# Kernel tuning notes

Measured on AMD Instinct MI355X. Metric: run time of the kernel, lower is better.

Reference implementation:

```python
import jax, jax.numpy as jnp
import numpy as np

NUM_NEIGHBORS = 10
BN_EPS = 1e-5


def setup_inputs() -> dict:
    key = jax.random.key(0)
    ks = jax.random.split(key, 6)
    B, N, D = 8, 4096, 64
    x = jax.random.normal(ks[0], (B, N, D), jnp.float32)

    def w(k, shape):
        return jax.random.normal(k, shape, jnp.float32) * 0.05

    return {
        "x": x,
        "gamma": jnp.ones((D,), jnp.float32),
        "beta": jnp.zeros((D,), jnp.float32),
        "W1": w(ks[1], (128, 128)), "b1": jnp.zeros((128,), jnp.float32),
        "W2": w(ks[2], (128, 64)), "b2": jnp.zeros((64,), jnp.float32),
        "W3": w(ks[3], (64, 64)), "b3": jnp.zeros((64,), jnp.float32),
        "Wg": w(ks[4], (128, 64)), "bg": jnp.zeros((64,), jnp.float32),
    }


def reference(x, gamma, beta, W1, b1, W2, b2, W3, b3, Wg, bg):
    B, N, D = x.shape
    K = NUM_NEIGHBORS

    # BatchNorm1d in train mode: normalize over all B*N rows with batch stats
    xf = x.reshape(-1, D)
    mu = jnp.mean(xf, axis=0)
    var = jnp.mean((xf - mu) ** 2, axis=0)  # biased, as torch BN uses
    xn = (((xf - mu) / jnp.sqrt(var + BN_EPS)) * gamma + beta).reshape(B, N, D)

    # KNN in feature space (standard DGCNN gather_neighbours)
    sq = jnp.sum(xn * xn, axis=-1)  # [B,N]
    dist = sq[:, :, None] + sq[:, None, :] - 2.0 * jnp.einsum("bnd,bmd->bnm", xn, xn)
    _, idx = jax.lax.top_k(-dist, K)  # [B,N,K] indices of nearest (incl. self)

    # gather neighbor features: neigh[b,n,k,:] = xn[b, idx[b,n,k], :]
    neigh = jax.vmap(lambda f, i: f[i])(xn, idx)  # [B,N,K,D]

    exp = jnp.broadcast_to(xn[:, :, None, :], (B, N, K, D))
    edge = jnp.concatenate([exp, exp - neigh], axis=-1)  # [B,N,K,2D]

    h = jax.nn.relu(edge @ W1 + b1)
    h = jax.nn.relu(h @ W2 + b2)
    h = jax.nn.relu(h @ W3 + b3)  # [B,N,K,64]

    vert = jnp.max(h, axis=2)  # max over neighbors -> [B,N,64]
    g = jnp.max(vert, axis=1, keepdims=True)  # global max-pool [B,1,64]
    cat = jnp.concatenate([vert, jnp.broadcast_to(g, vert.shape)], axis=-1)  # [B,N,128]
    return jax.nn.relu(cat @ Wg + bg)  # [B,N,64]
```

## Files before the change

### kernel.cpp

```cpp
#include <hip/hip_runtime.h>
#include <hip/hip_fp16.h>
#include <float.h>

#define BB 8
#define NN 4096
#define DD 64
#define KNBR 10
#define ROWS (BB*NN)

typedef _Float16 f16x8 __attribute__((ext_vector_type(8)));
typedef float f32x4 __attribute__((ext_vector_type(4)));

__global__ void k_bn_stats(const float* __restrict__ x, float* __restrict__ stats) {
  __shared__ float ls[2][4][64];
  int d = threadIdx.x & 63;
  int g = threadIdx.x >> 6;
  float s = 0.f, s2 = 0.f;
  for (int r = blockIdx.x * 4 + g; r < ROWS; r += gridDim.x * 4) {
    float val = x[r * 64 + d];
    s += val;
    s2 = fmaf(val, val, s2);
  }
  ls[0][g][d] = s;
  ls[1][g][d] = s2;
  __syncthreads();
  if (g == 0) {
    atomicAdd(&stats[d],      ls[0][0][d] + ls[0][1][d] + ls[0][2][d] + ls[0][3][d]);
    atomicAdd(&stats[64 + d], ls[1][0][d] + ls[1][1][d] + ls[1][2][d] + ls[1][3][d]);
  }
}

__global__ void k_bn_finalize(const float* __restrict__ stats,
                              const float* __restrict__ gamma,
                              const float* __restrict__ beta,
                              float* __restrict__ ss) {
  int d = threadIdx.x;
  const float inv = 1.f / 32768.f;
  float mu  = stats[d] * inv;
  float var = stats[64 + d] * inv - mu * mu;
  float sc  = gamma[d] / sqrtf(var + 1e-5f);
  ss[d]      = sc;
  ss[64 + d] = beta[d] - mu * sc;
}

__global__ void k_normalize(const float* __restrict__ x, const float* __restrict__ ss,
                            float* __restrict__ xn, float* __restrict__ sq,
                            _Float16* __restrict__ xh, _Float16* __restrict__ xl) {
  int row = blockIdx.x * 4 + (threadIdx.x >> 6);
  int d = threadIdx.x & 63;
  int idx = row * 64 + d;
  float val = fmaf(x[idx], ss[d], ss[64 + d]);
  xn[idx] = val;
  _Float16 h = (_Float16)val;
  _Float16 l = (_Float16)(val - (float)h);
  xh[idx] = h;
  xl[idx] = l;
  float p = val * val;
  #pragma unroll
  for (int off = 32; off > 0; off >>= 1) p += __shfl_xor(p, off);
  if (d == 0) sq[row] = p;
}

__global__ __launch_bounds__(256, 2) void k_knn(const _Float16* __restrict__ xh,
                                                const _Float16* __restrict__ xl,
                                                const float* __restrict__ sq,
                                                int* __restrict__ knn) {
  __shared__ __align__(16) float lds[16640];
  __shared__ float thrs[64];
  __shared__ int cnts[64];
  const int tid = threadIdx.x;
  const int w = tid >> 6, lane = tid & 63;
  const int l15 = lane & 15, lg = lane >> 4;
  const int b = blockIdx.x >> 6;
  const int rowbase = (blockIdx.x & 63) << 6;
  const int bN = b * NN;
  const _Float16* __restrict__ xhb = xh + (size_t)bN * 64;
  const _Float16* __restrict__ xlb = xl + (size_t)bN * 64;

  char* wbase = (char*)lds + w * 16640;
  char* Bhi = wbase;
  char* Blo = wbase + 4096;
  float* Dw = (float*)(wbase + 8192);

  f16x8 Ah[4][2], Al[4][2];
  #pragma unroll
  for (int mt = 0; mt < 4; ++mt) {
    #pragma unroll
    for (int ks = 0; ks < 2; ++ks) {
      int r = rowbase + mt * 16 + l15;
      Ah[mt][ks] = *(const f16x8*)(xhb + r * 64 + ks * 32 + lg * 8);
      Al[mt][ks] = *(const f16x8*)(xlb + r * 64 + ks * 32 + lg * 8);
    }
  }

  float bd[10];
  #pragma unroll
  for (int i = 0; i < 10; ++i) bd[i] = FLT_MAX;

  int srow[4], scc[4];
  #pragma unroll
  for (int i = 0; i < 4; ++i) { int c = i * 64 + lane; srow[i] = c >> 3; scc[i] = c & 7; }

  f16x8 sh[4], sl[4];
  {
    int mb0 = w * 32;
    #pragma unroll
    for (int i = 0; i < 4; ++i) {
      sh[i] = *(const f16x8*)(xhb + (mb0 + srow[i]) * 64 + scc[i] * 8);
      sl[i] = *(const f16x8*)(xlb + (mb0 + srow[i]) * 64 + scc[i] * 8);
    }
  }

  float* Drow = Dw + lane * 33;

  #pragma unroll 1
  for (int t = 0; t < 32; ++t) {
    const int mb = (t * 4 + w) * 32;
    const int mb2 = (t < 31) ? ((t + 1) * 4 + w) * 32 : mb;
    float sqv0 = sq[bN + mb + l15];
    float sqv1 = sq[bN + mb + 16 + l15];
    #pragma unroll
    for (int i = 0; i < 4; ++i) {
      int off = srow[i] * 128 + 16 * (scc[i] ^ (srow[i] & 7));
      *(f16x8*)(Bhi + off) = sh[i];
      *(f16x8*)(Blo + off) = sl[i];
    }
    #pragma unroll
    for (int i = 0; i < 4; ++i) {
      sh[i] = *(const f16x8*)(xhb + (mb2 + srow[i]) * 64 + scc[i] * 8);
      sl[i] = *(const f16x8*)(xlb + (mb2 + srow[i]) * 64 + scc[i] * 8);
    }
    f16x8 Bh[2][2], Bl[2][2];
    #pragma unroll
    for (int nt = 0; nt < 2; ++nt) {
      #pragma unroll
      for (int ks = 0; ks < 2; ++ks) {
        int rr2 = nt * 16 + l15;
        int off = rr2 * 128 + 16 * ((ks * 4 + lg) ^ (rr2 & 7));
        Bh[nt][ks] = *(const f16x8*)(Bhi + off);
        Bl[nt][ks] = *(const f16x8*)(Blo + off);
      }
    }
    #pragma unroll
    for (int mt = 0; mt < 4; ++mt) {
      f32x4 a0 = {0.f, 0.f, 0.f, 0.f}, a1 = {0.f, 0.f, 0.f, 0.f};
      #pragma unroll
      for (int ks = 0; ks < 2; ++ks) {
        a0 = __builtin_amdgcn_mfma_f32_16x16x32_f16(Ah[mt][ks], Bh[0][ks], a0, 0, 0, 0);
        a1 = __builtin_amdgcn_mfma_f32_16x16x32_f16(Ah[mt][ks], Bh[1][ks], a1, 0, 0, 0);
        a0 = __builtin_amdgcn_mfma_f32_16x16x32_f16(Ah[mt][ks], Bl[0][ks], a0, 0, 0, 0);
        a1 = __builtin_amdgcn_mfma_f32_16x16x32_f16(Ah[mt][ks], Bl[1][ks], a1, 0, 0, 0);
        a0 = __builtin_amdgcn_mfma_f32_16x16x32_f16(Al[mt][ks], Bh[0][ks], a0, 0, 0, 0);
        a1 = __builtin_amdgcn_mfma_f32_16x16x32_f16(Al[mt][ks], Bh[1][ks], a1, 0, 0, 0);
      }
      int rw = mt * 16 + lg * 4;
      #pragma unroll
      for (int r2 = 0; r2 < 4; ++r2) {
        Dw[(rw + r2) * 33 + l15]      = fmaf(-2.f, a0[r2], sqv0);
        Dw[(rw + r2) * 33 + 16 + l15] = fmaf(-2.f, a1[r2], sqv1);
      }
    }
    #pragma unroll 4
    for (int mm = 0; mm < 32; ++mm) {
      float cd = Drow[mm];
      if (cd < bd[9]) {
        float prev = bd[0];
        bd[0] = fminf(cd, bd[0]);
        #pragma unroll
        for (int j = 1; j < 10; ++j) {
          float cur = bd[j];
          bd[j] = fminf(cur, fmaxf(prev, cd));
          prev = cur;
        }
      }
    }
  }

  __syncthreads();
  float* md = lds;
  #pragma unroll
  for (int i = 0; i < 10; ++i) md[(w * 64 + lane) * 10 + i] = bd[i];
  if (tid < 64) cnts[tid] = 0;
  __syncthreads();
  if (tid < 64) {
    float fd[10];
    #pragma unroll
    for (int i = 0; i < 10; ++i) fd[i] = FLT_MAX;
    for (int w2 = 0; w2 < 4; ++w2) {
      #pragma unroll
      for (int kk = 0; kk < 10; ++kk) {
        float cd = md[(w2 * 64 + tid) * 10 + kk];
        if (cd < fd[9]) {
          float prev = fd[0];
          fd[0] = fminf(cd, fd[0]);
          #pragma unroll
          for (int j = 1; j < 10; ++j) {
            float cur = fd[j];
            fd[j] = fminf(cur, fmaxf(prev, cd));
            prev = cur;
          }
        }
      }
    }
    thrs[tid] = fd[9];
  }
  __syncthreads();

  float thv[4][4];
  #pragma unroll
  for (int mt = 0; mt < 4; ++mt)
    #pragma unroll
    for (int r2 = 0; r2 < 4; ++r2)
      thv[mt][r2] = thrs[mt * 16 + lg * 4 + r2];

  int* knnrow = knn + (size_t)(bN + rowbase) * KNBR;

  {
    int mb0 = w * 32;
    #pragma unroll
    for (int i = 0; i < 4; ++i) {
      sh[i] = *(const f16x8*)(xhb + (mb0 + srow[i]) * 64 + scc[i] * 8);
      sl[i] = *(const f16x8*)(xlb + (mb0 + srow[i]) * 64 + scc[i] * 8);
    }
  }
  #pragma unroll 1
  for (int t = 0; t < 32; ++t) {
    const int mb = (t * 4 + w) * 32;
    const int mb2 = (t < 31) ? ((t + 1) * 4 + w) * 32 : mb;
    float sqv0 = sq[bN + mb + l15];
    float sqv1 = sq[bN + mb + 16 + l15];
    #pragma unroll
    for (int i = 0; i < 4; ++i) {
      int off = srow[i] * 128 + 16 * (scc[i] ^ (srow[i] & 7));
      *(f16x8*)(Bhi + off) = sh[i];
      *(f16x8*)(Blo + off) = sl[i];
    }
    #pragma unroll
    for (int i = 0; i < 4; ++i) {
      sh[i] = *(const f16x8*)(xhb + (mb2 + srow[i]) * 64 + scc[i] * 8);
      sl[i] = *(const f16x8*)(xlb + (mb2 + srow[i]) * 64 + scc[i] * 8);
    }
    f16x8 Bh[2][2], Bl[2][2];
    #pragma unroll
    for (int nt = 0; nt < 2; ++nt) {
      #pragma unroll
      for (int ks = 0; ks < 2; ++ks) {
        int rr2 = nt * 16 + l15;
        int off = rr2 * 128 + 16 * ((ks * 4 + lg) ^ (rr2 & 7));
        Bh[nt][ks] = *(const f16x8*)(Bhi + off);
        Bl[nt][ks] = *(const f16x8*)(Blo + off);
      }
    }
    #pragma unroll
    for (int mt = 0; mt < 4; ++mt) {
      f32x4 a0 = {0.f, 0.f, 0.f, 0.f}, a1 = {0.f, 0.f, 0.f, 0.f};
      #pragma unroll
      for (int ks = 0; ks < 2; ++ks) {
        a0 = __builtin_amdgcn_mfma_f32_16x16x32_f16(Ah[mt][ks], Bh[0][ks], a0, 0, 0, 0);
        a1 = __builtin_amdgcn_mfma_f32_16x16x32_f16(Ah[mt][ks], Bh[1][ks], a1, 0, 0, 0);
        a0 = __builtin_amdgcn_mfma_f32_16x16x32_f16(Ah[mt][ks], Bl[0][ks], a0, 0, 0, 0);
        a1 = __builtin_amdgcn_mfma_f32_16x16x32_f16(Ah[mt][ks], Bl[1][ks], a1, 0, 0, 0);
        a0 = __builtin_amdgcn_mfma_f32_16x16x32_f16(Al[mt][ks], Bh[0][ks], a0, 0, 0, 0);
        a1 = __builtin_amdgcn_mfma_f32_16x16x32_f16(Al[mt][ks], Bh[1][ks], a1, 0, 0, 0);
      }
      #pragma unroll
      for (int r2 = 0; r2 < 4; ++r2) {
        float d0 = fmaf(-2.f, a0[r2], sqv0);
        float d1 = fmaf(-2.f, a1[r2], sqv1);
        int row = mt * 16 + lg * 4 + r2;
        if (d0 <= thv[mt][r2]) {
          int slot = atomicAdd(&cnts[row], 1);
          if (slot < KNBR) knnrow[row * KNBR + slot] = bN + mb + l15;
        }
        if (d1 <= thv[mt][r2]) {
          int slot = atomicAdd(&cnts[row], 1);
          if (slot < KNBR) knnrow[row * KNBR + slot] = bN + mb + 16 + l15;
        }
      }
    }
  }
}

__global__ void k_uv(const float* __restrict__ xn, const float* __restrict__ W1,
                     const float* __restrict__ b1, _Float16* __restrict__ u,
                     _Float16* __restrict__ v) {
  __shared__ float xs[64 * 64];
  const int tid = threadIdx.x;
  const int o = tid & 127;
  const bool isU = tid < 128;
  const int rowbase = blockIdx.x * 64;

  float wreg[64];
  #pragma unroll
  for (int d = 0; d < 64; ++d) {
    float bw = W1[(64 + d) * 128 + o];
    wreg[d] = isU ? (W1[d * 128 + o] + bw) : bw;
  }
  const float bb = isU ? b1[o] : 0.f;
  _Float16* __restrict__ dst = isU ? u : v;

  {
    const float4* s4 = (const float4*)(xn + rowbase * 64);
    float4* d4 = (float4*)xs;
    #pragma unroll
    for (int i = 0; i < 4; ++i) d4[tid + 256 * i] = s4[tid + 256 * i];
  }
  __syncthreads();

  for (int r = 0; r < 64; ++r) {
    const float4* xr = (const float4*)(xs + r * 64);
    float a0 = bb, a1 = 0.f, a2 = 0.f, a3 = 0.f;
    #pragma unroll
    for (int q = 0; q < 16; ++q) {
      float4 xv = xr[q];
      a0 = fmaf(xv.x, wreg[4 * q + 0], a0);
      a1 = fmaf(xv.y, wreg[4 * q + 1], a1);
      a2 = fmaf(xv.z, wreg[4 * q + 2], a2);
      a3 = fmaf(xv.w, wreg[4 * q + 3], a3);
    }
    dst[(rowbase + r) * 128 + o] = (_Float16)((a0 + a1) + (a2 + a3));
  }
}

__global__ __launch_bounds__(256, 2) void k_edge(const _Float16* __restrict__ uu,
                                                 const _Float16* __restrict__ vv,
                                                 const int* __restrict__ knn,
                                                 const float* __restrict__ W2,
                                                 const float* __restrict__ b2,
                                                 const float* __restrict__ W3,
                                                 const float* __restrict__ b3,
                                                 float* __restrict__ vert) {
  __shared__ __align__(16) _Float16 W3Ts[64 * 72];
  __shared__ __align__(16) _Float16 h2buf[4][16 * 88];
  __shared__ int vmaxs[4][512];
  const int tid = threadIdx.x;
  const int w = tid >> 6, lane = tid & 63;
  const int l15 = lane & 15, lg = lane >> 4;

  for (int i = tid; i < 64 * 64; i += 256) {
    int o3 = i >> 6, k2 = i & 63;
    W3Ts[o3 * 72 + k2] = (_Float16)W3[k2 * 64 + o3];
  }
  f16x8 w2f[4][4];
  #pragma unroll
  for (int ks = 0; ks < 4; ++ks) {
    #pragma unroll
    for (int nt = 0; nt < 4; ++nt) {
      f16x8 t;
      #pragma unroll
      for (int j = 0; j < 8; ++j)
        t[j] = (_Float16)W2[(ks * 32 + lg * 8 + j) * 64 + nt * 16 + l15];
      w2f[ks][nt] = t;
    }
  }
  float bias2[4], bias3[4];
  #pragma unroll
  for (int nt = 0; nt < 4; ++nt) { bias2[nt] = b2[nt * 16 + l15]; bias3[nt] = b3[nt * 16 + l15]; }

  _Float16* h2w = h2buf[w];
  int* vmaxw = vmaxs[w];
  #pragma unroll
  for (int q = 0; q < 8; ++q) vmaxw[lane * 8 + q] = 0;
  __syncthreads();

  const int g = blockIdx.x * 4 + w;
  const int n0 = g * 8;
  const int ebase = n0 * KNBR;
  #pragma unroll 1
  for (int mt = 0; mt < 5; ++mt) {
    const int e = mt * 16 + l15;
    const int m = knn[ebase + e];
    const int n = n0 + e / 10;
    const _Float16* Up = uu + (size_t)n * 128 + lg * 8;
    const _Float16* Vp = vv + (size_t)m * 128 + lg * 8;
    f16x8 A[4];
    #pragma unroll
    for (int ks = 0; ks < 4; ++ks) {
      f16x8 ud = *(const f16x8*)(Up + ks * 32);
      f16x8 vd = *(const f16x8*)(Vp + ks * 32);
      f16x8 df = ud - vd;
      f16x8 t;
      #pragma unroll
      for (int j = 0; j < 8; ++j)
        t[j] = df[j] > (_Float16)0.f ? df[j] : (_Float16)0.f;
      A[ks] = t;
    }
    f32x4 acc[4];
    #pragma unroll
    for (int nt = 0; nt < 4; ++nt) { float bbv = bias2[nt]; acc[nt] = (f32x4){bbv, bbv, bbv, bbv}; }
    #pragma unroll
    for (int ks = 0; ks < 4; ++ks) {
      #pragma unroll
      for (int nt = 0; nt < 4; ++nt)
        acc[nt] = __builtin_amdgcn_mfma_f32_16x16x32_f16(A[ks], w2f[ks][nt], acc[nt], 0, 0, 0);
    }
    #pragma unroll
    for (int nt = 0; nt < 4; ++nt) {
      #pragma unroll
      for (int r = 0; r < 4; ++r)
        h2w[(lg * 4 + r) * 88 + nt * 16 + l15] = (_Float16)fmaxf(acc[nt][r], 0.f);
    }
    f16x8 A3[2];
    #pragma unroll
    for (int ks2 = 0; ks2 < 2; ++ks2)
      A3[ks2] = *(const f16x8*)(h2w + l15 * 88 + ks2 * 32 + lg * 8);
    f32x4 c3[4];
    #pragma unroll
    for (int nt = 0; nt < 4; ++nt) { float bbv = bias3[nt]; c3[nt] = (f32x4){bbv, bbv, bbv, bbv}; }
    #pragma unroll
    for (int ks2 = 0; ks2 < 2; ++ks2) {
      #pragma unroll
      for (int nt = 0; nt < 4; ++nt) {
        f16x8 bf = *(const f16x8*)(W3Ts + (nt * 16 + l15) * 72 + ks2 * 32 + lg * 8);
        c3[nt] = __builtin_amdgcn_mfma_f32_16x16x32_f16(A3[ks2], bf, c3[nt], 0, 0, 0);
      }
    }
    #pragma unroll
    for (int nt = 0; nt < 4; ++nt) {
      #pragma unroll
      for (int r = 0; r < 4; ++r) {
        float val = fmaxf(c3[nt][r], 0.f);
        int e2 = mt * 16 + lg * 4 + r;
        int p = e2 / 10;
        atomicMax(&vmaxw[p * 64 + nt * 16 + l15], __float_as_int(val));
      }
    }
  }
  {
    int p2 = lane >> 3, c0 = (lane & 7) * 8;
    const int* vp = &vmaxw[p2 * 64 + c0];
    float4 r0, r1;
    r0.x = __int_as_float(vp[0]); r0.y = __int_as_float(vp[1]);
    r0.z = __int_as_float(vp[2]); r0.w = __int_as_float(vp[3]);
    r1.x = __int_as_float(vp[4]); r1.y = __int_as_float(vp[5]);
    r1.z = __int_as_float(vp[6]); r1.w = __int_as_float(vp[7]);
    *(float4*)(vert + (size_t)(n0 + p2) * 64 + c0) = r0;
    *(float4*)(vert + (size_t)(n0 + p2) * 64 + c0 + 4) = r1;
  }
}

__global__ void k_gmax(const float* __restrict__ vert, float* __restrict__ g) {
  __shared__ float red[4][64];
  int b = blockIdx.x >> 4, chunk = blockIdx.x & 15;
  int sub = threadIdx.x >> 6, o = threadIdx.x & 63;
  float vm = 0.f;
  for (int j = 0; j < 64; ++j) {
    int r = chunk * 256 + j * 4 + sub;
    vm = fmaxf(vm, vert[(b * NN + r) * 64 + o]);
  }
  red[sub][o] = vm;
  __syncthreads();
  if (sub == 0) {
    float mm = fmaxf(fmaxf(red[0][o], red[1][o]), fmaxf(red[2][o], red[3][o]));
    atomicMax((int*)&g[b * 64 + o], __float_as_int(mm));
  }
}

__global__ void k_gb(const float* __restrict__ g, const float* __restrict__ Wg,
                     const float* __restrict__ bg, float* __restrict__ gb) {
  int t = threadIdx.x;
  int b = t >> 6, o = t & 63;
  float acc = bg[o];
  #pragma unroll
  for (int i = 0; i < 64; ++i)
    acc = fmaf(g[b * 64 + i], Wg[(64 + i) * 64 + o], acc);
  gb[b * 64 + o] = acc;
}

__global__ void k_final(const float* __restrict__ vert, const float* __restrict__ Wg,
                        const float* __restrict__ gb, float* __restrict__ out) {
  __shared__ float Wgs[64 * 64];
  int tid = threadIdx.x, w = tid >> 6, lane = tid & 63;
  for (int i = tid; i < 4096; i += 256) Wgs[i] = Wg[i];
  __syncthreads();
  int gw = blockIdx.x * 4 + w;
  for (int j = 0; j < 4; ++j) {
    int n = gw + 8192 * j;
    int b = n >> 12;
    float vrow = vert[n * 64 + lane];
    float ac0 = gb[b * 64 + lane], ac1 = 0.f, ac2 = 0.f, ac3 = 0.f;
    #pragma unroll
    for (int i = 0; i < 64; i += 4) {
      ac0 = fmaf(__shfl(vrow, i),     Wgs[i * 64 + lane],       ac0);
      ac1 = fmaf(__shfl(vrow, i + 1), Wgs[(i + 1) * 64 + lane], ac1);
      ac2 = fmaf(__shfl(vrow, i + 2), Wgs[(i + 2) * 64 + lane], ac2);
      ac3 = fmaf(__shfl(vrow, i + 3), Wgs[(i + 3) * 64 + lane], ac3);
    }
    out[n * 64 + lane] = fmaxf((ac0 + ac1) + (ac2 + ac3), 0.f);
  }
}

extern "C" void kernel_launch(void* const* d_in, const int* in_sizes, int n_in,
                              void* d_out, int out_size, void* d_ws, size_t ws_size,
                              hipStream_t stream) {
  const float* x     = (const float*)d_in[0];
  const float* gamma = (const float*)d_in[1];
  const float* beta  = (const float*)d_in[2];
  const float* W1    = (const float*)d_in[3];
  const float* b1    = (const float*)d_in[4];
  const float* W2    = (const float*)d_in[5];
  const float* b2    = (const float*)d_in[6];
  const float* W3    = (const float*)d_in[7];
  const float* b3    = (const float*)d_in[8];
  const float* Wg    = (const float*)d_in[9];
  const float* bg    = (const float*)d_in[10];
  float* out = (float*)d_out;

  float* ws    = (float*)d_ws;
  float* stats = ws;
  float* ss    = ws + 128;
  float* xn    = ws + 256;
  float* sq    = xn + 2097152;
  int*   knn   = (int*)(sq + 32768);
  _Float16* u  = (_Float16*)(knn + 327680);
  _Float16* v  = u + 4194304;
  float* vert  = (float*)(v + 4194304);
  float* g     = vert + 2097152;
  float* gb    = g + 512;
  _Float16* xh = (_Float16*)(gb + 512);
  _Float16* xl = (_Float16*)(gb + 512 + 1048576);

  hipMemsetAsync(stats, 0, 128 * sizeof(float), stream);
  hipMemsetAsync(g, 0, 512 * sizeof(float), stream);

  k_bn_stats<<<256, 256, 0, stream>>>(x, stats);
  k_bn_finalize<<<1, 64, 0, stream>>>(stats, gamma, beta, ss);
  k_normalize<<<8192, 256, 0, stream>>>(x, ss, xn, sq, xh, xl);
  k_knn<<<512, 256, 0, stream>>>(xh, xl, sq, knn);
  k_uv<<<512, 256, 0, stream>>>(xn, W1, b1, u, v);
  k_edge<<<1024, 256, 0, stream>>>(u, v, knn, W2, b2, W3, b3, vert);
  k_gmax<<<128, 256, 0, stream>>>(vert, g);
  k_gb<<<1, 512, 0, stream>>>(g, Wg, bg, gb);
  k_final<<<2048, 256, 0, stream>>>(vert, Wg, gb, out);
}
```

Before: 459.7 us.

## Fuse global max-pool into edge kernel and global bias into final kernel

The per-batch global max over vertex features is now reduced in shared memory inside the edge kernel and pushed with one atomicMax per channel per block, which removes the separate gmax kernel and its re-read of vert. The global-feature projection (g @ Wg bottom half + bg) is recomputed in every final-kernel block instead of in a dedicated single-block kernel. Two launches go away, at the cost of extra shared atomics in the edge kernel and 512x64 redundant FMAs per final block.

```diff
diff --git a/kernel.cpp b/kernel.cpp
--- a/kernel.cpp
+++ b/kernel.cpp
@@ -329,10 +329,12 @@
                                                  const float* __restrict__ b2,
                                                  const float* __restrict__ W3,
                                                  const float* __restrict__ b3,
-                                                 float* __restrict__ vert) {
+                                                 float* __restrict__ vert,
+                                                 float* __restrict__ gmax) {
   __shared__ __align__(16) _Float16 W3Ts[64 * 72];
   __shared__ __align__(16) _Float16 h2buf[4][16 * 88];
   __shared__ int vmaxs[4][512];
+  __shared__ int gblk[64];
   const int tid = threadIdx.x;
   const int w = tid >> 6, lane = tid & 63;
   const int l15 = lane & 15, lg = lane >> 4;
@@ -361,6 +363,7 @@
   int* vmaxw = vmaxs[w];
   #pragma unroll
   for (int q = 0; q < 8; ++q) vmaxw[lane * 8 + q] = 0;
+  if (tid < 64) gblk[tid] = 0;
   __syncthreads();
 
   const int g = blockIdx.x * 4 + w;
@@ -436,49 +439,44 @@
     r1.z = __int_as_float(vp[6]); r1.w = __int_as_float(vp[7]);
     *(float4*)(vert + (size_t)(n0 + p2) * 64 + c0) = r0;
     *(float4*)(vert + (size_t)(n0 + p2) * 64 + c0 + 4) = r1;
-  }
-}
-
-__global__ void k_gmax(const float* __restrict__ vert, float* __restrict__ g) {
-  __shared__ float red[4][64];
-  int b = blockIdx.x >> 4, chunk = blockIdx.x & 15;
-  int sub = threadIdx.x >> 6, o = threadIdx.x & 63;
-  float vm = 0.f;
-  for (int j = 0; j < 64; ++j) {
-    int r = chunk * 256 + j * 4 + sub;
-    vm = fmaxf(vm, vert[(b * NN + r) * 64 + o]);
-  }
-  red[sub][o] = vm;
-  __syncthreads();
-  if (sub == 0) {
-    float mm = fmaxf(fmaxf(red[0][o], red[1][o]), fmaxf(red[2][o], red[3][o]));
-    atomicMax((int*)&g[b * 64 + o], __float_as_int(mm));
-  }
-}
-
-__global__ void k_gb(const float* __restrict__ g, const float* __restrict__ Wg,
-                     const float* __restrict__ bg, float* __restrict__ gb) {
-  int t = threadIdx.x;
-  int b = t >> 6, o = t & 63;
-  float acc = bg[o];
-  #pragma unroll
-  for (int i = 0; i < 64; ++i)
-    acc = fmaf(g[b * 64 + i], Wg[(64 + i) * 64 + o], acc);
-  gb[b * 64 + o] = acc;
+    atomicMax(&gblk[c0 + 0], __float_as_int(r0.x));
+    atomicMax(&gblk[c0 + 1], __float_as_int(r0.y));
+    atomicMax(&gblk[c0 + 2], __float_as_int(r0.z));
+    atomicMax(&gblk[c0 + 3], __float_as_int(r0.w));
+    atomicMax(&gblk[c0 + 4], __float_as_int(r1.x));
+    atomicMax(&gblk[c0 + 5], __float_as_int(r1.y));
+    atomicMax(&gblk[c0 + 6], __float_as_int(r1.z));
+    atomicMax(&gblk[c0 + 7], __float_as_int(r1.w));
+  }
+  __syncthreads();
+  if (tid < 64) {
+    int bb2 = (blockIdx.x * 32) >> 12;
+    atomicMax((int*)&gmax[bb2 * 64 + tid], gblk[tid]);
+  }
 }
 
 __global__ void k_final(const float* __restrict__ vert, const float* __restrict__ Wg,
-                        const float* __restrict__ gb, float* __restrict__ out) {
+                        const float* __restrict__ bg, const float* __restrict__ gmax,
+                        float* __restrict__ out) {
   __shared__ float Wgs[64 * 64];
+  __shared__ float gbs[8 * 64];
   int tid = threadIdx.x, w = tid >> 6, lane = tid & 63;
   for (int i = tid; i < 4096; i += 256) Wgs[i] = Wg[i];
+  for (int t2 = tid; t2 < 512; t2 += 256) {
+    int b_ = t2 >> 6, o = t2 & 63;
+    float acc = bg[o];
+    #pragma unroll
+    for (int i = 0; i < 64; ++i)
+      acc = fmaf(gmax[b_ * 64 + i], Wg[(64 + i) * 64 + o], acc);
+    gbs[t2] = acc;
+  }
   __syncthreads();
   int gw = blockIdx.x * 4 + w;
   for (int j = 0; j < 4; ++j) {
     int n = gw + 8192 * j;
     int b = n >> 12;
     float vrow = vert[n * 64 + lane];
-    float ac0 = gb[b * 64 + lane], ac1 = 0.f, ac2 = 0.f, ac3 = 0.f;
+    float ac0 = gbs[b * 64 + lane], ac1 = 0.f, ac2 = 0.f, ac3 = 0.f;
     #pragma unroll
     for (int i = 0; i < 64; i += 4) {
       ac0 = fmaf(__shfl(vrow, i),     Wgs[i * 64 + lane],       ac0);
@@ -516,9 +514,8 @@
   _Float16* v  = u + 4194304;
   float* vert  = (float*)(v + 4194304);
   float* g     = vert + 2097152;
-  float* gb    = g + 512;
-  _Float16* xh = (_Float16*)(gb + 512);
-  _Float16* xl = (_Float16*)(gb + 512 + 1048576);
+  _Float16* xh = (_Float16*)(g + 512);
+  _Float16* xl = (_Float16*)(g + 512 + 1048576);
 
   hipMemsetAsync(stats, 0, 128 * sizeof(float), stream);
   hipMemsetAsync(g, 0, 512 * sizeof(float), stream);
@@ -528,8 +525,6 @@
   k_normalize<<<8192, 256, 0, stream>>>(x, ss, xn, sq, xh, xl);
   k_knn<<<512, 256, 0, stream>>>(xh, xl, sq, knn);
   k_uv<<<512, 256, 0, stream>>>(xn, W1, b1, u, v);
-  k_edge<<<1024, 256, 0, stream>>>(u, v, knn, W2, b2, W3, b3, vert);
-  k_gmax<<<128, 256, 0, stream>>>(vert, g);
-  k_gb<<<1, 512, 0, stream>>>(g, Wg, bg, gb);
-  k_final<<<2048, 256, 0, stream>>>(vert, Wg, gb, out);
-}
+  k_edge<<<1024, 256, 0, stream>>>(u, v, knn, W2, b2, W3, b3, vert, g);
+  k_final<<<2048, 256, 0, stream>>>(vert, Wg, bg, g, out);
+}
```

New measurement: 447.3 us (median of 2 runs). 2.7% less time.
